# Performance work log

Measured on AMD Instinct MI355X. Metric: run time of the kernel, lower is better.

## Reference

```python
import jax, jax.numpy as jnp
import numpy as np

N = 10000
D_IN = 512
D_OUT = 512
EDGE_P = 0.003  # ~30 avg degree


def setup_inputs() -> dict:
    key = jax.random.key(0)
    k_x, k_a, k_w1, k_b1, k_w2, k_b2 = jax.random.split(key, 6)
    x = jax.random.normal(k_x, (N, D_IN), dtype=jnp.float32)
    # sparse-ish binary adjacency, zero diagonal (GCNConv adds self-loops itself)
    adjacency = (jax.random.uniform(k_a, (N, N)) < EDGE_P).astype(jnp.float32)
    adjacency = adjacency * (1.0 - jnp.eye(N, dtype=jnp.float32))
    s1 = 1.0 / np.sqrt(D_IN)
    s2 = 1.0 / np.sqrt(D_OUT)
    W1 = jax.random.normal(k_w1, (D_IN, D_OUT), dtype=jnp.float32) * s1
    b1 = jax.random.normal(k_b1, (D_OUT,), dtype=jnp.float32) * 0.01
    W2 = jax.random.normal(k_w2, (D_OUT, D_OUT), dtype=jnp.float32) * s2
    b2 = jax.random.normal(k_b2, (D_OUT,), dtype=jnp.float32) * 0.01
    return {"x": x, "adjacency": adjacency, "W1": W1, "b1": b1, "W2": W2, "b2": b2}


def _gcn_norm(adjacency):
    # GCNConv gcn_norm: add self-loops (weight 1), deg = sum of incoming edge
    # weights at target (column sums), norm[i,j] = d_i^{-1/2} * Ahat[i,j] * d_j^{-1/2}
    n = adjacency.shape[0]
    Ahat = adjacency + jnp.eye(n, dtype=adjacency.dtype)
    deg = Ahat.sum(axis=0)
    dinv = jnp.where(deg > 0, deg ** -0.5, 0.0)
    return dinv[:, None] * Ahat * dinv[None, :]


def reference(x, adjacency, W1, b1, W2, b2):
    An = _gcn_norm(adjacency)  # [N, N]
    # out[j] = sum_i An[i,j] * (x W)[i]  ->  An.T @ (x W)
    h = jax.nn.relu(An.T @ (x @ W1) + b1)
    h = jax.nn.relu(An.T @ (h @ W2) + b2)
    return h
```

## Files before the change

kernel.cpp:

```cpp
#include <hip/hip_runtime.h>
#include <hip/hip_bf16.h>
#include <hip/hip_fp16.h>

#define N_NODES 10000
#define DFEAT 512
#define MPAD 10112
#define MAXDEG 96
#define NB_SPLITX 5056
#define NB_WSPLIT 512
#define NB_ZERO 40
#define GEMM_BLOCKS 316
#define NB_SCAN 10000

typedef __attribute__((ext_vector_type(8))) short short8x;
typedef __attribute__((ext_vector_type(4))) float f32x4;
typedef __attribute__((ext_vector_type(4))) _Float16 half4x;

__device__ __forceinline__ ushort f2bf(float f) {
    uint u = __builtin_bit_cast(uint, f);
    uint r = (u + 0x7FFFu + ((u >> 16) & 1u)) >> 16;
    return (ushort)r;
}
__device__ __forceinline__ float bf2f(ushort h) {
    uint u = ((uint)h) << 16;
    return __builtin_bit_cast(float, u);
}

typedef const __attribute__((address_space(1))) void gv_t;
typedef __attribute__((address_space(3))) void sv_t;
__device__ __forceinline__ void gload16(const void* g, void* l) {
    __builtin_amdgcn_global_load_lds((gv_t*)g, (sv_t*)l, 16, 0, 0);
}

__global__ __launch_bounds__(256) void prep_split(const float* __restrict__ X,
                                                  const float* __restrict__ W1,
                                                  const float* __restrict__ W2,
                                                  ushort* __restrict__ Ah,
                                                  ushort* __restrict__ Al,
                                                  ushort* __restrict__ W1hT,
                                                  ushort* __restrict__ W1lT,
                                                  ushort* __restrict__ W2hT,
                                                  ushort* __restrict__ W2lT,
                                                  int* __restrict__ cursor) {
    const int bid = blockIdx.x;
    const int tid = threadIdx.x;
    if (bid < NB_SPLITX) {
        size_t idx = (size_t)bid * 256 + tid;
        int row = (int)(idx >> 7);
        float4 v = make_float4(0.f, 0.f, 0.f, 0.f);
        if (row < N_NODES) v = ((const float4*)X)[idx];
        ushort4 hi, lo;
        hi.x = f2bf(v.x); lo.x = f2bf(v.x - bf2f(hi.x));
        hi.y = f2bf(v.y); lo.y = f2bf(v.y - bf2f(hi.y));
        hi.z = f2bf(v.z); lo.z = f2bf(v.z - bf2f(hi.z));
        hi.w = f2bf(v.w); lo.w = f2bf(v.w - bf2f(hi.w));
        ((ushort4*)Ah)[idx] = hi;
        ((ushort4*)Al)[idx] = lo;
    } else if (bid < NB_SPLITX + NB_WSPLIT) {
        __shared__ float tile[32][33];
        int wb = bid - NB_SPLITX;
        const float* W = (wb < 256) ? W1 : W2;
        ushort* WhT = (wb < 256) ? W1hT : W2hT;
        ushort* WlT = (wb < 256) ? W1lT : W2lT;
        int wi = wb & 255;
        int n0 = (wi & 15) * 32, k0 = (wi >> 4) * 32;
        const int tx = tid & 31, ty = tid >> 5;
#pragma unroll
        for (int p = 0; p < 4; ++p)
            tile[ty + p * 8][tx] = W[(size_t)(k0 + ty + p * 8) * DFEAT + n0 + tx];
        __syncthreads();
#pragma unroll
        for (int p = 0; p < 4; ++p) {
            int n = n0 + ty + p * 8;
            int k = k0 + tx;
            float v = tile[tx][ty + p * 8];
            ushort h = f2bf(v);
            WhT[(size_t)n * DFEAT + k] = h;
            WlT[(size_t)n * DFEAT + k] = f2bf(v - bf2f(h));
        }
    } else {
        int j = (bid - NB_SPLITX - NB_WSPLIT) * 256 + tid;
        if (j < N_NODES) cursor[j] = 0;
    }
}

template <bool PRE>
__device__ __forceinline__ void gemm_tile(const ushort* __restrict__ Ah,
                                          const ushort* __restrict__ Al,
                                          const ushort* __restrict__ BhT,
                                          const ushort* __restrict__ BlT,
                                          const int* __restrict__ cnt,
                                          _Float16* __restrict__ C, int M,
                                          int row0, int col0, int tid) {
    __shared__ ushort lAh[128 * 64];
    __shared__ ushort lAl[128 * 64];
    __shared__ ushort lBh[128 * 64];
    __shared__ ushort lBl[128 * 64];
    const int lane = tid & 63, wv = tid >> 6;
    const int wm = wv >> 1, wn = wv & 1;
    const int l15 = lane & 15, lg = lane >> 4;

    f32x4 acc[4][4];
#pragma unroll
    for (int i = 0; i < 4; ++i)
#pragma unroll
        for (int j = 0; j < 4; ++j) acc[i][j] = (f32x4){0.f, 0.f, 0.f, 0.f};

    for (int k0 = 0; k0 < 512; k0 += 64) {
#pragma unroll
        for (int c = 0; c < 4; ++c) {
            int o = wv * 4096 + c * 1024 + lane * 16;
            int r = o >> 7;
            int kb = (o & 127) ^ ((r & 7) << 4);
            size_t ga = (size_t)(row0 + r) * 1024 + (size_t)(k0 * 2) + kb;
            size_t gb = (size_t)(col0 + r) * 1024 + (size_t)(k0 * 2) + kb;
            int ldst = o - lane * 16;
            gload16((const char*)Ah + ga, (char*)lAh + ldst);
            gload16((const char*)Al + ga, (char*)lAl + ldst);
            gload16((const char*)BhT + gb, (char*)lBh + ldst);
            gload16((const char*)BlT + gb, (char*)lBl + ldst);
        }
        __syncthreads();

#pragma unroll
        for (int s = 0; s < 2; ++s) {
            short8x a_h[4], a_l[4], b_h[4], b_l[4];
#pragma unroll
            for (int i = 0; i < 4; ++i) {
                int r = wm * 64 + i * 16 + l15;
                int kbs = (s * 64 + 16 * lg) ^ ((r & 7) << 4);
                a_h[i] = *(const short8x*)((const char*)lAh + r * 128 + kbs);
                a_l[i] = *(const short8x*)((const char*)lAl + r * 128 + kbs);
            }
#pragma unroll
            for (int j = 0; j < 4; ++j) {
                int n = wn * 64 + j * 16 + l15;
                int kbs = (s * 64 + 16 * lg) ^ ((n & 7) << 4);
                b_h[j] = *(const short8x*)((const char*)lBh + n * 128 + kbs);
                b_l[j] = *(const short8x*)((const char*)lBl + n * 128 + kbs);
            }
#pragma unroll
            for (int i = 0; i < 4; ++i)
#pragma unroll
                for (int j = 0; j < 4; ++j) {
                    acc[i][j] = __builtin_amdgcn_mfma_f32_16x16x32_bf16(a_h[i], b_h[j], acc[i][j], 0, 0, 0);
                    acc[i][j] = __builtin_amdgcn_mfma_f32_16x16x32_bf16(a_h[i], b_l[j], acc[i][j], 0, 0, 0);
                    acc[i][j] = __builtin_amdgcn_mfma_f32_16x16x32_bf16(a_l[i], b_h[j], acc[i][j], 0, 0, 0);
                }
        }
        __syncthreads();
    }

#pragma unroll
    for (int i = 0; i < 4; ++i) {
#pragma unroll
        for (int r = 0; r < 4; ++r) {
            int grow = row0 + wm * 64 + i * 16 + lg * 4 + r;
            if (grow < M) {
                float dv = 1.0f;
                if (PRE) dv = 1.0f / sqrtf((float)cnt[grow] + 1.0f);
#pragma unroll
                for (int j = 0; j < 4; ++j) {
                    int gcol = col0 + wn * 64 + j * 16 + l15;
                    C[(size_t)grow * DFEAT + gcol] = (_Float16)(dv * acc[i][j][r]);
                }
            }
        }
    }
}

__global__ __launch_bounds__(256, 2) void mega_gemm_scan(const ushort* __restrict__ Ah,
                                                         const ushort* __restrict__ Al,
                                                         const ushort* __restrict__ BhT,
                                                         const ushort* __restrict__ BlT,
                                                         _Float16* __restrict__ C,
                                                         const float* __restrict__ A,
                                                         int* __restrict__ cursor,
                                                         int* __restrict__ slot) {
    const int bid = blockIdx.x;
    if (bid < GEMM_BLOCKS) {
        gemm_tile<false>(Ah, Al, BhT, BlT, nullptr, C, N_NODES,
                         (bid >> 2) * 128, (bid & 3) * 128, threadIdx.x);
    } else {
        const int row = bid - GEMM_BLOCKS;
        const int tid = threadIdx.x;
        const float4* Arow = (const float4*)(A + (size_t)row * N_NODES);
        for (int c = tid; c < N_NODES / 4; c += 256) {
            float4 v = Arow[c];
            float vv[4] = {v.x, v.y, v.z, v.w};
#pragma unroll
            for (int k = 0; k < 4; ++k) {
                if (vv[k] != 0.0f) {
                    int j = c * 4 + k;
                    int pos = atomicAdd(&cursor[j], 1);
                    if (pos < MAXDEG) slot[j * MAXDEG + pos] = row;
                }
            }
        }
    }
}

__global__ __launch_bounds__(256, 2) void gemm2(const ushort* __restrict__ Ah,
                                                const ushort* __restrict__ Al,
                                                const ushort* __restrict__ BhT,
                                                const ushort* __restrict__ BlT,
                                                const int* __restrict__ cursor,
                                                _Float16* __restrict__ C) {
    gemm_tile<true>(Ah, Al, BhT, BlT, cursor, C, N_NODES,
                    (blockIdx.x >> 2) * 128, (blockIdx.x & 3) * 128, threadIdx.x);
}

__global__ __launch_bounds__(128) void agg1(const _Float16* __restrict__ G,
                                            const int* __restrict__ cursor,
                                            const int* __restrict__ slot,
                                            const float* __restrict__ bias,
                                            ushort* __restrict__ Hh,
                                            ushort* __restrict__ Hl) {
    const int j = blockIdx.x;
    const int tid = threadIdx.x;
    __shared__ int sidx[MAXDEG];
    __shared__ float sw[MAXDEG];
    const half4x* G4 = (const half4x*)G;
    const int cj = cursor[j];
    const int cnt = min(cj, MAXDEG);
    if (tid < cnt) {
        int i = slot[j * MAXDEG + tid];
        sidx[tid] = i;
        sw[tid] = 1.0f / sqrtf((float)cursor[i] + 1.0f);
    }
    __syncthreads();
    const float dj = 1.0f / sqrtf((float)cj + 1.0f);
    half4x h = G4[(j << 7) + tid];
    float4 acc = make_float4(dj * (float)h[0], dj * (float)h[1],
                             dj * (float)h[2], dj * (float)h[3]);
    int c = 0;
    for (; c + 8 <= cnt; c += 8) {
        half4x u[8];
        float w[8];
#pragma unroll
        for (int q = 0; q < 8; ++q) { u[q] = G4[(sidx[c + q] << 7) + tid]; w[q] = sw[c + q]; }
#pragma unroll
        for (int q = 0; q < 8; ++q) {
            acc.x += w[q] * (float)u[q][0]; acc.y += w[q] * (float)u[q][1];
            acc.z += w[q] * (float)u[q][2]; acc.w += w[q] * (float)u[q][3];
        }
    }
    for (; c < cnt; ++c) {
        half4x u = G4[(sidx[c] << 7) + tid];
        float w = sw[c];
        acc.x += w * (float)u[0]; acc.y += w * (float)u[1];
        acc.z += w * (float)u[2]; acc.w += w * (float)u[3];
    }
    float4 b = ((const float4*)bias)[tid];
    float4 o;
    o.x = fmaxf(dj * acc.x + b.x, 0.0f);
    o.y = fmaxf(dj * acc.y + b.y, 0.0f);
    o.z = fmaxf(dj * acc.z + b.z, 0.0f);
    o.w = fmaxf(dj * acc.w + b.w, 0.0f);
    ushort4 hi, lo;
    hi.x = f2bf(o.x); lo.x = f2bf(o.x - bf2f(hi.x));
    hi.y = f2bf(o.y); lo.y = f2bf(o.y - bf2f(hi.y));
    hi.z = f2bf(o.z); lo.z = f2bf(o.z - bf2f(hi.z));
    hi.w = f2bf(o.w); lo.w = f2bf(o.w - bf2f(hi.w));
    ((ushort4*)(Hh + ((size_t)j << 9)))[tid] = hi;
    ((ushort4*)(Hl + ((size_t)j << 9)))[tid] = lo;
}

__global__ __launch_bounds__(128) void agg2(const _Float16* __restrict__ G,
                                            const int* __restrict__ cursor,
                                            const int* __restrict__ slot,
                                            const float* __restrict__ bias,
                                            float* __restrict__ out) {
    const int j = blockIdx.x;
    const int tid = threadIdx.x;
    __shared__ int sidx[MAXDEG];
    const half4x* G4 = (const half4x*)G;
    const int cj = cursor[j];
    const int cnt = min(cj, MAXDEG);
    if (tid < cnt) sidx[tid] = slot[j * MAXDEG + tid];
    __syncthreads();
    half4x h = G4[(j << 7) + tid];
    float4 acc = make_float4((float)h[0], (float)h[1], (float)h[2], (float)h[3]);
    int c = 0;
    for (; c + 8 <= cnt; c += 8) {
        half4x u[8];
#pragma unroll
        for (int q = 0; q < 8; ++q) u[q] = G4[(sidx[c + q] << 7) + tid];
#pragma unroll
        for (int q = 0; q < 8; ++q) {
            acc.x += (float)u[q][0]; acc.y += (float)u[q][1];
            acc.z += (float)u[q][2]; acc.w += (float)u[q][3];
        }
    }
    for (; c < cnt; ++c) {
        half4x u = G4[(sidx[c] << 7) + tid];
        acc.x += (float)u[0]; acc.y += (float)u[1];
        acc.z += (float)u[2]; acc.w += (float)u[3];
    }
    const float dj = 1.0f / sqrtf((float)cj + 1.0f);
    float4 b = ((const float4*)bias)[tid];
    float4 o;
    o.x = fmaxf(dj * acc.x + b.x, 0.0f);
    o.y = fmaxf(dj * acc.y + b.y, 0.0f);
    o.z = fmaxf(dj * acc.z + b.z, 0.0f);
    o.w = fmaxf(dj * acc.w + b.w, 0.0f);
    ((float4*)(out + ((size_t)j << 9)))[tid] = o;
}

extern "C" void kernel_launch(void* const* d_in, const int* in_sizes, int n_in,
                              void* d_out, int out_size, void* d_ws, size_t ws_size,
                              hipStream_t stream) {
    const float* x  = (const float*)d_in[0];
    const float* A  = (const float*)d_in[1];
    const float* W1 = (const float*)d_in[2];
    const float* b1 = (const float*)d_in[3];
    const float* W2 = (const float*)d_in[4];
    const float* b2 = (const float*)d_in[5];
    float* out = (float*)d_out;

    char* ws = (char*)d_ws;
    size_t off = 0;
    auto alloc = [&](size_t bytes) -> void* {
        void* p = ws + off;
        off = (off + bytes + 255) & ~(size_t)255;
        return p;
    };
    _Float16* XW16 = (_Float16*)alloc((size_t)MPAD * DFEAT * 2);
    ushort* Ah   = (ushort*)alloc((size_t)MPAD * DFEAT * 2);
    ushort* Al   = (ushort*)alloc((size_t)MPAD * DFEAT * 2);
    ushort* Hh   = (ushort*)alloc((size_t)MPAD * DFEAT * 2);
    ushort* Hl   = (ushort*)alloc((size_t)MPAD * DFEAT * 2);
    ushort* W1hT = (ushort*)alloc((size_t)DFEAT * DFEAT * 2);
    ushort* W1lT = (ushort*)alloc((size_t)DFEAT * DFEAT * 2);
    ushort* W2hT = (ushort*)alloc((size_t)DFEAT * DFEAT * 2);
    ushort* W2lT = (ushort*)alloc((size_t)DFEAT * DFEAT * 2);
    int*  cursor = (int*)alloc((size_t)N_NODES * 4);
    int*    slot = (int*)alloc((size_t)N_NODES * MAXDEG * 4);

    prep_split<<<NB_SPLITX + NB_WSPLIT + NB_ZERO, 256, 0, stream>>>(
        x, W1, W2, Ah, Al, W1hT, W1lT, W2hT, W2lT, cursor);

    mega_gemm_scan<<<GEMM_BLOCKS + NB_SCAN, 256, 0, stream>>>(
        Ah, Al, W1hT, W1lT, XW16, A, cursor, slot);

    agg1<<<N_NODES, 128, 0, stream>>>(XW16, cursor, slot, b1, Hh, Hl);

    gemm2<<<GEMM_BLOCKS, 256, 0, stream>>>(Hh, Hl, W2hT, W2lT, cursor, XW16);

    agg2<<<N_NODES, 128, 0, stream>>>(XW16, cursor, slot, b2, out);
}
```

Baseline: 764.7 us.

## Halve GEMM K-tile for higher occupancy, batch adjacency scan loads, memset cursor

The GEMM K-step drops from 64 to 32, which halves shared memory per block and uses a new 4-way XOR swizzle. Launch bounds rise from 2 to 4 blocks per SM so more waves can hide latency. The adjacency scan now issues all ten float4 row loads up front before testing for nonzeros, giving more memory-level parallelism. Cursor zeroing moves from extra prep blocks to a hipMemsetAsync call, and the smaller K-step doubles the number of barrier syncs per tile.

```diff
diff --git a/kernel.cpp b/kernel.cpp
--- a/kernel.cpp
+++ b/kernel.cpp
@@ -8,7 +8,6 @@
 #define MAXDEG 96
 #define NB_SPLITX 5056
 #define NB_WSPLIT 512
-#define NB_ZERO 40
 #define GEMM_BLOCKS 316
 #define NB_SCAN 10000
 
@@ -40,8 +39,7 @@
                                                   ushort* __restrict__ W1hT,
                                                   ushort* __restrict__ W1lT,
                                                   ushort* __restrict__ W2hT,
-                                                  ushort* __restrict__ W2lT,
-                                                  int* __restrict__ cursor) {
+                                                  ushort* __restrict__ W2lT) {
     const int bid = blockIdx.x;
     const int tid = threadIdx.x;
     if (bid < NB_SPLITX) {
@@ -56,7 +54,7 @@
         hi.w = f2bf(v.w); lo.w = f2bf(v.w - bf2f(hi.w));
         ((ushort4*)Ah)[idx] = hi;
         ((ushort4*)Al)[idx] = lo;
-    } else if (bid < NB_SPLITX + NB_WSPLIT) {
+    } else {
         __shared__ float tile[32][33];
         int wb = bid - NB_SPLITX;
         const float* W = (wb < 256) ? W1 : W2;
@@ -78,9 +76,6 @@
             WhT[(size_t)n * DFEAT + k] = h;
             WlT[(size_t)n * DFEAT + k] = f2bf(v - bf2f(h));
         }
-    } else {
-        int j = (bid - NB_SPLITX - NB_WSPLIT) * 256 + tid;
-        if (j < N_NODES) cursor[j] = 0;
     }
 }
 
@@ -92,10 +87,10 @@
                                           const int* __restrict__ cnt,
                                           _Float16* __restrict__ C, int M,
                                           int row0, int col0, int tid) {
-    __shared__ ushort lAh[128 * 64];
-    __shared__ ushort lAl[128 * 64];
-    __shared__ ushort lBh[128 * 64];
-    __shared__ ushort lBl[128 * 64];
+    __shared__ ushort lAh[128 * 32];
+    __shared__ ushort lAl[128 * 32];
+    __shared__ ushort lBh[128 * 32];
+    __shared__ ushort lBl[128 * 32];
     const int lane = tid & 63, wv = tid >> 6;
     const int wm = wv >> 1, wn = wv & 1;
     const int l15 = lane & 15, lg = lane >> 4;
@@ -106,48 +101,44 @@
 #pragma unroll
         for (int j = 0; j < 4; ++j) acc[i][j] = (f32x4){0.f, 0.f, 0.f, 0.f};
 
-    for (int k0 = 0; k0 < 512; k0 += 64) {
-#pragma unroll
-        for (int c = 0; c < 4; ++c) {
-            int o = wv * 4096 + c * 1024 + lane * 16;
-            int r = o >> 7;
-            int kb = (o & 127) ^ ((r & 7) << 4);
-            size_t ga = (size_t)(row0 + r) * 1024 + (size_t)(k0 * 2) + kb;
-            size_t gb = (size_t)(col0 + r) * 1024 + (size_t)(k0 * 2) + kb;
-            int ldst = o - lane * 16;
-            gload16((const char*)Ah + ga, (char*)lAh + ldst);
-            gload16((const char*)Al + ga, (char*)lAl + ldst);
-            gload16((const char*)BhT + gb, (char*)lBh + ldst);
-            gload16((const char*)BlT + gb, (char*)lBl + ldst);
+    for (int k0 = 0; k0 < 512; k0 += 32) {
+#pragma unroll
+        for (int c = 0; c < 2; ++c) {
+            int o = (wv * 2 + c) * 1024 + lane * 16;
+            int r = o >> 6;
+            int gsl = ((o >> 4) & 3) ^ (r & 3);
+            size_t ga = (size_t)(row0 + r) * 1024 + (size_t)(k0 * 2) + gsl * 16;
+            size_t gb = (size_t)(col0 + r) * 1024 + (size_t)(k0 * 2) + gsl * 16;
+            gload16((const char*)Ah + ga, (char*)lAh + o);
+            gload16((const char*)Al + ga, (char*)lAl + o);
+            gload16((const char*)BhT + gb, (char*)lBh + o);
+            gload16((const char*)BlT + gb, (char*)lBl + o);
         }
         __syncthreads();
 
-#pragma unroll
-        for (int s = 0; s < 2; ++s) {
-            short8x a_h[4], a_l[4], b_h[4], b_l[4];
-#pragma unroll
-            for (int i = 0; i < 4; ++i) {
-                int r = wm * 64 + i * 16 + l15;
-                int kbs = (s * 64 + 16 * lg) ^ ((r & 7) << 4);
-                a_h[i] = *(const short8x*)((const char*)lAh + r * 128 + kbs);
-                a_l[i] = *(const short8x*)((const char*)lAl + r * 128 + kbs);
+        short8x a_h[4], a_l[4], b_h[4], b_l[4];
+#pragma unroll
+        for (int i = 0; i < 4; ++i) {
+            int r = wm * 64 + i * 16 + l15;
+            int bo = r * 64 + ((lg ^ (r & 3)) << 4);
+            a_h[i] = *(const short8x*)((const char*)lAh + bo);
+            a_l[i] = *(const short8x*)((const char*)lAl + bo);
+        }
+#pragma unroll
+        for (int j = 0; j < 4; ++j) {
+            int n = wn * 64 + j * 16 + l15;
+            int bo = n * 64 + ((lg ^ (n & 3)) << 4);
+            b_h[j] = *(const short8x*)((const char*)lBh + bo);
+            b_l[j] = *(const short8x*)((const char*)lBl + bo);
+        }
+#pragma unroll
+        for (int i = 0; i < 4; ++i)
+#pragma unroll
+            for (int j = 0; j < 4; ++j) {
+                acc[i][j] = __builtin_amdgcn_mfma_f32_16x16x32_bf16(a_h[i], b_h[j], acc[i][j], 0, 0, 0);
+                acc[i][j] = __builtin_amdgcn_mfma_f32_16x16x32_bf16(a_h[i], b_l[j], acc[i][j], 0, 0, 0);
+                acc[i][j] = __builtin_amdgcn_mfma_f32_16x16x32_bf16(a_l[i], b_h[j], acc[i][j], 0, 0, 0);
             }
-#pragma unroll
-            for (int j = 0; j < 4; ++j) {
-                int n = wn * 64 + j * 16 + l15;
-                int kbs = (s * 64 + 16 * lg) ^ ((n & 7) << 4);
-                b_h[j] = *(const short8x*)((const char*)lBh + n * 128 + kbs);
-                b_l[j] = *(const short8x*)((const char*)lBl + n * 128 + kbs);
-            }
-#pragma unroll
-            for (int i = 0; i < 4; ++i)
-#pragma unroll
-                for (int j = 0; j < 4; ++j) {
-                    acc[i][j] = __builtin_amdgcn_mfma_f32_16x16x32_bf16(a_h[i], b_h[j], acc[i][j], 0, 0, 0);
-                    acc[i][j] = __builtin_amdgcn_mfma_f32_16x16x32_bf16(a_h[i], b_l[j], acc[i][j], 0, 0, 0);
-                    acc[i][j] = __builtin_amdgcn_mfma_f32_16x16x32_bf16(a_l[i], b_h[j], acc[i][j], 0, 0, 0);
-                }
-        }
         __syncthreads();
     }
 
@@ -169,7 +160,7 @@
     }
 }
 
-__global__ __launch_bounds__(256, 2) void mega_gemm_scan(const ushort* __restrict__ Ah,
+__global__ __launch_bounds__(256, 4) void mega_gemm_scan(const ushort* __restrict__ Ah,
                                                          const ushort* __restrict__ Al,
                                                          const ushort* __restrict__ BhT,
                                                          const ushort* __restrict__ BlT,
@@ -185,9 +176,14 @@
         const int row = bid - GEMM_BLOCKS;
         const int tid = threadIdx.x;
         const float4* Arow = (const float4*)(A + (size_t)row * N_NODES);
-        for (int c = tid; c < N_NODES / 4; c += 256) {
-            float4 v = Arow[c];
-            float vv[4] = {v.x, v.y, v.z, v.w};
+        float4 v[10];
+#pragma unroll
+        for (int q = 0; q < 9; ++q) v[q] = Arow[tid + q * 256];
+        v[9] = (tid < 2500 - 2304) ? Arow[tid + 2304] : make_float4(0.f, 0.f, 0.f, 0.f);
+#pragma unroll
+        for (int q = 0; q < 10; ++q) {
+            int c = tid + q * 256;
+            float vv[4] = {v[q].x, v[q].y, v[q].z, v[q].w};
 #pragma unroll
             for (int k = 0; k < 4; ++k) {
                 if (vv[k] != 0.0f) {
@@ -200,7 +196,7 @@
     }
 }
 
-__global__ __launch_bounds__(256, 2) void gemm2(const ushort* __restrict__ Ah,
+__global__ __launch_bounds__(256, 4) void gemm2(const ushort* __restrict__ Ah,
                                                 const ushort* __restrict__ Al,
                                                 const ushort* __restrict__ BhT,
                                                 const ushort* __restrict__ BlT,
@@ -337,8 +333,10 @@
     int*  cursor = (int*)alloc((size_t)N_NODES * 4);
     int*    slot = (int*)alloc((size_t)N_NODES * MAXDEG * 4);
 
-    prep_split<<<NB_SPLITX + NB_WSPLIT + NB_ZERO, 256, 0, stream>>>(
-        x, W1, W2, Ah, Al, W1hT, W1lT, W2hT, W2lT, cursor);
+    hipMemsetAsync(cursor, 0, (size_t)N_NODES * 4, stream);
+
+    prep_split<<<NB_SPLITX + NB_WSPLIT, 256, 0, stream>>>(
+        x, W1, W2, Ah, Al, W1hT, W1lT, W2hT, W2lT);
 
     mega_gemm_scan<<<GEMM_BLOCKS + NB_SCAN, 256, 0, stream>>>(
         Ah, Al, W1hT, W1lT, XW16, A, cursor, slot);
```

Result: faster. 658.2 us (-13.9%).
